# Optimization experiments

Hardware: AMD Instinct MI355X
Metric: run time of the kernel (lower is better)

The kernel has to match this reference:

```python
import jax, jax.numpy as jnp
import numpy as np

B, L, D, H, DFF, MAXD = 4, 2048, 1024, 16, 4096, 512
HD = D // H


def layer_norm(x, gamma, beta, eps=1e-5):
    mu = jnp.mean(x, axis=-1, keepdims=True)
    var = jnp.mean(jnp.square(x - mu), axis=-1, keepdims=True)
    return (x - mu) * jax.lax.rsqrt(var + eps) * gamma + beta


def setup_inputs() -> dict:
    key = jax.random.key(0)
    ks = jax.random.split(key, 8)
    s = 0.02
    return {
        "x": jax.random.normal(ks[0], (B, L, D), jnp.float32),
        "w_qkv": jax.random.normal(ks[1], (D, 3 * D), jnp.float32) * s,
        "w_out": jax.random.normal(ks[2], (D, D), jnp.float32) * s,
        "b_out": jnp.zeros((D,), jnp.float32),
        "bias_table": jax.random.normal(ks[3], (2 * MAXD - 1, H), jnp.float32) * s,
        "gamma1": jnp.ones((D,), jnp.float32),
        "beta1": jnp.zeros((D,), jnp.float32),
        "w_ff1": jax.random.normal(ks[4], (D, DFF), jnp.float32) * s,
        "b_ff1": jnp.zeros((DFF,), jnp.float32),
        "w_ff2": jax.random.normal(ks[5], (DFF, D), jnp.float32) * s,
        "b_ff2": jnp.zeros((D,), jnp.float32),
        "gamma2": jnp.ones((D,), jnp.float32),
        "beta2": jnp.zeros((D,), jnp.float32),
    }


def reference(x, w_qkv, w_out, b_out, bias_table, gamma1, beta1,
              w_ff1, b_ff1, w_ff2, b_ff2, gamma2, beta2):
    b, l, c = x.shape
    scale = HD ** -0.5
    qkv = x @ w_qkv  # [B,L,3D]
    q, k, v = jnp.split(qkv, 3, axis=-1)
    # [B,H,L,hd]
    q = q.reshape(b, l, H, HD).transpose(0, 2, 1, 3)
    k = k.reshape(b, l, H, HD).transpose(0, 2, 1, 3)
    v = v.reshape(b, l, H, HD).transpose(0, 2, 1, 3)
    scores = jnp.einsum("bhqd,bhkd->bhqk", q, k) * scale
    # relative position bias: [H,L,L]
    coords = jnp.arange(l)
    rel = jnp.clip(coords[None, :] - coords[:, None] + MAXD - 1, 0, 2 * MAXD - 2)
    bias = bias_table[rel].transpose(2, 0, 1)
    scores = scores + bias[None]
    attn = jax.nn.softmax(scores, axis=-1)
    ctx = jnp.einsum("bhqk,bhkd->bhqd", attn, v)
    ctx = ctx.transpose(0, 2, 1, 3).reshape(b, l, c)
    attn_out = ctx @ w_out + b_out
    x = layer_norm(x + attn_out, gamma1, beta1)
    h = jax.nn.gelu(x @ w_ff1 + b_ff1, approximate=False)
    ffn_out = h @ w_ff2 + b_ff2
    x = layer_norm(x + ffn_out, gamma2, beta2)
    return x
```

## Files before the change

### kernel.cpp

```cpp
#include <hip/hip_runtime.h>

typedef unsigned short u16;
typedef __bf16 bf16x8 __attribute__((ext_vector_type(8)));
typedef float f32x4 __attribute__((ext_vector_type(4)));
typedef unsigned short u16x8 __attribute__((ext_vector_type(8)));

typedef __attribute__((address_space(1))) const void gvoid_t;
typedef __attribute__((address_space(3))) void svoid_t;

__device__ __forceinline__ float bf2f(u16 u) {
  union { unsigned int i; float f; } v; v.i = ((unsigned int)u) << 16; return v.f;
}
__device__ __forceinline__ u16 f2bf(float f) {
  union { float f; unsigned int i; } v; v.f = f;
  unsigned int u = v.i;
  return (u16)((u + 0x7fffu + ((u >> 16) & 1u)) >> 16);
}
__device__ __forceinline__ void async_copy16(const u16* g, u16* l) {
  __builtin_amdgcn_global_load_lds((gvoid_t*)g, (svoid_t*)l, 16, 0, 0);
}
__device__ __forceinline__ f32x4 mfma16(bf16x8 a, bf16x8 b, f32x4 c) {
  return __builtin_amdgcn_mfma_f32_16x16x32_bf16(a, b, c, 0, 0, 0);
}

__global__ __launch_bounds__(256) void pack_bf16(const float* __restrict__ src, u16* __restrict__ dst, int n4) {
  int i = blockIdx.x * 256 + threadIdx.x;
  if (i >= n4) return;
  float4 v = *(const float4*)(src + (size_t)i * 4);
  ushort4 o;
  o.x = f2bf(v.x); o.y = f2bf(v.y); o.z = f2bf(v.z); o.w = f2bf(v.w);
  *(ushort4*)(dst + (size_t)i * 4) = o;
}

__global__ void transpose_f2b(const float* __restrict__ src, u16* __restrict__ dst, int R, int C) {
  __shared__ u16 t[32][33];
  const int c0 = blockIdx.x * 32, r0 = blockIdx.y * 32;
  const int tx = threadIdx.x, ty = threadIdx.y;
#pragma unroll
  for (int i = 0; i < 4; ++i) {
    int r = r0 + ty + i * 8;
    t[ty + i * 8][tx] = f2bf(src[(size_t)r * C + c0 + tx]);
  }
  __syncthreads();
#pragma unroll
  for (int i = 0; i < 4; ++i) {
    int c = c0 + ty + i * 8;
    dst[(size_t)c * R + r0 + tx] = t[tx][ty + i * 8];
  }
}

__global__ void transpose_v(const u16* __restrict__ qkv, u16* __restrict__ vT2) {
  __shared__ u16 t[32][33];
  const int bh = blockIdx.z;
  const int b = bh >> 4, h = bh & 15;
  const int l0 = blockIdx.x * 32, d0 = blockIdx.y * 32;
  const int tx = threadIdx.x, ty = threadIdx.y;
#pragma unroll
  for (int i = 0; i < 4; ++i) {
    int l = l0 + ty + i * 8;
    t[ty + i * 8][tx] = qkv[(size_t)(b * 2048 + l) * 3072 + 2048 + h * 64 + d0 + tx];
  }
  __syncthreads();
#pragma unroll
  for (int i = 0; i < 4; ++i) {
    int d = d0 + ty + i * 8;
    vT2[(size_t)bh * 131072 + (l0 >> 5) * 2048 + d * 32 + tx] = t[tx][ty + i * 8];
  }
}

template <int EPI>
__global__ __launch_bounds__(256) void gemm_bt(const u16* __restrict__ A, const u16* __restrict__ Bt,
                                               const float* __restrict__ bias, u16* __restrict__ C,
                                               int M, int N, int K) {
  __shared__ __align__(16) u16 As[128 * 32];
  __shared__ __align__(16) u16 Bs[128 * 32];
  const int tid = threadIdx.x;
  const int wave = tid >> 6, lane = tid & 63;
  const int quad = lane >> 4, l16 = lane & 15;
  const int wm = wave >> 1, wn = wave & 1;
  const int m0 = blockIdx.y * 128, n0 = blockIdx.x * 128;
  const int srow = lane >> 2, scol = (lane & 3) * 8;
  f32x4 acc[4][4] = {};
  for (int k0 = 0; k0 < K; k0 += 32) {
#pragma unroll
    for (int rr = 0; rr < 2; ++rr) {
      const int chunk = rr * 4 + wave;
      const int row = chunk * 16 + srow;
      async_copy16(&A[(size_t)(m0 + row) * K + k0 + scol], &As[chunk * 16 * 32]);
      async_copy16(&Bt[(size_t)(n0 + row) * K + k0 + scol], &Bs[chunk * 16 * 32]);
    }
    __syncthreads();
    bf16x8 af[4], bfv[4];
#pragma unroll
    for (int i = 0; i < 4; ++i)
      af[i] = *(const bf16x8*)&As[(wm * 64 + i * 16 + l16) * 32 + quad * 8];
#pragma unroll
    for (int j = 0; j < 4; ++j)
      bfv[j] = *(const bf16x8*)&Bs[(wn * 64 + j * 16 + l16) * 32 + quad * 8];
#pragma unroll
    for (int i = 0; i < 4; ++i)
#pragma unroll
      for (int j = 0; j < 4; ++j)
        acc[i][j] = mfma16(af[i], bfv[j], acc[i][j]);
    __syncthreads();
  }
#pragma unroll
  for (int i = 0; i < 4; ++i)
#pragma unroll
    for (int j = 0; j < 4; ++j) {
      const int col = n0 + wn * 64 + j * 16 + l16;
      float bv = 0.f;
      if (EPI > 0) bv = bias[col];
#pragma unroll
      for (int r = 0; r < 4; ++r) {
        const int row = m0 + wm * 64 + i * 16 + quad * 4 + r;
        float v = acc[i][j][r] + bv;
        if (EPI == 2) v = 0.5f * v * (1.f + erff(v * 0.70710678118654752f));
        C[(size_t)row * N + col] = f2bf(v);
      }
    }
}

__global__ __launch_bounds__(256) void attn_kernel(const u16* __restrict__ qkv, const u16* __restrict__ vT2,
                                                   const float* __restrict__ btab, u16* __restrict__ ctx) {
  const int tid = threadIdx.x;
  const int wave = tid >> 6, lane = tid & 63;
  const int quad = lane >> 4, l16 = lane & 15;
  const int bh = blockIdx.x >> 4, qb = blockIdx.x & 15;
  const int b = bh >> 4, h = bh & 15;
  const int q0b = qb * 128;
  const int qw = q0b + wave * 32;

  __shared__ __align__(16) u16 Ks[32 * 68];
  __shared__ __align__(16) u16 Vs[64 * 36];
  __shared__ __align__(16) float bias_s[160];
  __shared__ __align__(16) u16 P[4][2][16 * 36];

  bf16x8 qf[2][2];
#pragma unroll
  for (int qi = 0; qi < 2; ++qi)
#pragma unroll
    for (int kk = 0; kk < 2; ++kk) {
      const u16* qp = &qkv[((size_t)(b * 2048) + qw + qi * 16 + l16) * 3072 + h * 64 + kk * 32 + quad * 8];
      union { u16 s[8]; bf16x8 v; } u;
#pragma unroll
      for (int j = 0; j < 8; ++j) u.s[j] = f2bf(bf2f(qp[j]) * 0.125f);
      qf[qi][kk] = u.v;
    }

  f32x4 o[2][4] = {};
  float psum[2][4] = {};

  const float c_lo = btab[h], c_hi = btab[1022 * 16 + h];
  const int skey = tid >> 3, schunk = tid & 7;
  const int svd = tid >> 2, svc = tid & 3;

  for (int kt = 0; kt < 64; ++kt) {
    const int kbase = kt * 32;
    const int dmax = kbase - q0b + 31, dmin = kbase - q0b - 127;
    const int mode = (dmax <= -511) ? 1 : (dmin >= 511 ? 2 : 0);
    {
      u16x8 kv = *(const u16x8*)&qkv[((size_t)(b * 2048) + kbase + skey) * 3072 + 1024 + h * 64 + schunk * 8];
      *(u16x8*)&Ks[skey * 68 + schunk * 8] = kv;
      u16x8 vv = *(const u16x8*)&vT2[(size_t)bh * 131072 + kt * 2048 + tid * 8];
      *(u16x8*)&Vs[svd * 36 + svc * 8] = vv;
    }
    if (mode == 0 && tid < 160) {
      int d = dmin + tid + 511;
      d = min(max(d, 0), 1022);
      bias_s[tid] = btab[d * 16 + h];
    }
    __syncthreads();
    bf16x8 kf0[2], kf1[2];
#pragma unroll
    for (int t = 0; t < 2; ++t) {
      kf0[t] = *(const bf16x8*)&Ks[(t * 16 + l16) * 68 + quad * 8];
      kf1[t] = *(const bf16x8*)&Ks[(t * 16 + l16) * 68 + 32 + quad * 8];
    }
#pragma unroll
    for (int qi = 0; qi < 2; ++qi) {
      u16* pw = P[wave][qi];
#pragma unroll
      for (int t = 0; t < 2; ++t) {
        f32x4 z = {0.f, 0.f, 0.f, 0.f};
        z = mfma16(qf[qi][0], kf0[t], z);
        z = mfma16(qf[qi][1], kf1[t], z);
#pragma unroll
        for (int r = 0; r < 4; ++r) {
          float bv;
          if (mode == 1) bv = c_lo;
          else if (mode == 2) bv = c_hi;
          else bv = bias_s[t * 16 + l16 - (wave * 32 + qi * 16 + quad * 4 + r) + 127];
          float p = __expf(z[r] + bv);
          psum[qi][r] += p;
          union { float f; unsigned int i; } cv; cv.f = p;
          pw[(quad * 4 + r) * 36 + t * 16 + l16] = (u16)(cv.i >> 16);
        }
      }
    }
    bf16x8 pa0 = *(const bf16x8*)&P[wave][0][l16 * 36 + quad * 8];
    bf16x8 pa1 = *(const bf16x8*)&P[wave][1][l16 * 36 + quad * 8];
#pragma unroll
    for (int c = 0; c < 4; ++c) {
      bf16x8 vf = *(const bf16x8*)&Vs[(c * 16 + l16) * 36 + quad * 8];
      o[0][c] = mfma16(pa0, vf, o[0][c]);
      o[1][c] = mfma16(pa1, vf, o[1][c]);
    }
    __syncthreads();
  }
#pragma unroll
  for (int qi = 0; qi < 2; ++qi)
#pragma unroll
    for (int off = 1; off < 16; off <<= 1)
#pragma unroll
      for (int r = 0; r < 4; ++r) psum[qi][r] += __shfl_xor(psum[qi][r], off);
#pragma unroll
  for (int qi = 0; qi < 2; ++qi)
#pragma unroll
    for (int r = 0; r < 4; ++r) {
      float inv = 1.f / psum[qi][r];
      int row = qw + qi * 16 + quad * 4 + r;
#pragma unroll
      for (int c = 0; c < 4; ++c)
        ctx[((size_t)(b * 2048 + row)) * 1024 + h * 64 + c * 16 + l16] = f2bf(o[qi][c][r] * inv);
    }
}

template <int A_F32, int O_F32>
__global__ __launch_bounds__(256) void add_ln(const void* __restrict__ av, const u16* __restrict__ b,
                                              const float* __restrict__ gamma, const float* __restrict__ beta,
                                              void* __restrict__ ov) {
  const int row = blockIdx.x, t = threadIdx.x;
  const size_t base = (size_t)row * 1024 + t * 4;
  float x0, x1, x2, x3;
  if (A_F32) {
    float4 a4 = *(const float4*)((const float*)av + base);
    x0 = a4.x; x1 = a4.y; x2 = a4.z; x3 = a4.w;
  } else {
    ushort4 a4 = *(const ushort4*)((const u16*)av + base);
    x0 = bf2f(a4.x); x1 = bf2f(a4.y); x2 = bf2f(a4.z); x3 = bf2f(a4.w);
  }
  ushort4 b4 = *(const ushort4*)&b[base];
  x0 += bf2f(b4.x); x1 += bf2f(b4.y); x2 += bf2f(b4.z); x3 += bf2f(b4.w);
  float s = x0 + x1 + x2 + x3;
  float q = x0 * x0 + x1 * x1 + x2 * x2 + x3 * x3;
  for (int off = 32; off > 0; off >>= 1) { s += __shfl_down(s, off); q += __shfl_down(q, off); }
  __shared__ float sh_s[4], sh_q[4];
  if ((t & 63) == 0) { sh_s[t >> 6] = s; sh_q[t >> 6] = q; }
  __syncthreads();
  s = sh_s[0] + sh_s[1] + sh_s[2] + sh_s[3];
  q = sh_q[0] + sh_q[1] + sh_q[2] + sh_q[3];
  float mu = s * (1.f / 1024.f);
  float var = q * (1.f / 1024.f) - mu * mu;
  float rs = rsqrtf(var + 1e-5f);
  float4 g4 = *(const float4*)&gamma[t * 4];
  float4 be4 = *(const float4*)&beta[t * 4];
  float y0 = (x0 - mu) * rs * g4.x + be4.x;
  float y1 = (x1 - mu) * rs * g4.y + be4.y;
  float y2 = (x2 - mu) * rs * g4.z + be4.z;
  float y3 = (x3 - mu) * rs * g4.w + be4.w;
  if (O_F32) {
    float4 o4 = {y0, y1, y2, y3};
    *(float4*)((float*)ov + base) = o4;
  } else {
    ushort4 o4;
    o4.x = f2bf(y0); o4.y = f2bf(y1); o4.z = f2bf(y2); o4.w = f2bf(y3);
    *(ushort4*)((u16*)ov + base) = o4;
  }
}

extern "C" void kernel_launch(void* const* d_in, const int* in_sizes, int n_in,
                              void* d_out, int out_size, void* d_ws, size_t ws_size,
                              hipStream_t stream) {
  const float* x      = (const float*)d_in[0];
  const float* w_qkv  = (const float*)d_in[1];
  const float* w_out  = (const float*)d_in[2];
  const float* b_out  = (const float*)d_in[3];
  const float* btab   = (const float*)d_in[4];
  const float* gamma1 = (const float*)d_in[5];
  const float* beta1  = (const float*)d_in[6];
  const float* w_ff1  = (const float*)d_in[7];
  const float* b_ff1  = (const float*)d_in[8];
  const float* w_ff2  = (const float*)d_in[9];
  const float* b_ff2  = (const float*)d_in[10];
  const float* gamma2 = (const float*)d_in[11];
  const float* beta2  = (const float*)d_in[12];
  float* out = (float*)d_out;

  char* w = (char*)d_ws;
  auto alloc = [&](size_t elems) { u16* p = (u16*)w; w += elems * 2; return p; };
  u16* wqkvT = alloc(3072UL * 1024);
  u16* woutT = alloc(1024UL * 1024);
  u16* wff1T = alloc(4096UL * 1024);
  u16* wff2T = alloc(1024UL * 4096);
  u16* xb    = alloc(8192UL * 1024);
  u16* qkv   = alloc(8192UL * 3072);
  u16* vT2   = alloc(64UL * 64 * 2048);
  u16* ctx   = alloc(8192UL * 1024);
  u16* x1    = alloc(8192UL * 1024);
  u16* attn  = qkv;
  u16* h     = qkv;
  u16* ffn   = ctx;

  dim3 tb(32, 8);
  pack_bf16<<<8192, 256, 0, stream>>>(x, xb, 8192 * 1024 / 4);
  transpose_f2b<<<dim3(3072 / 32, 1024 / 32), tb, 0, stream>>>(w_qkv, wqkvT, 1024, 3072);
  transpose_f2b<<<dim3(1024 / 32, 1024 / 32), tb, 0, stream>>>(w_out, woutT, 1024, 1024);
  transpose_f2b<<<dim3(4096 / 32, 1024 / 32), tb, 0, stream>>>(w_ff1, wff1T, 1024, 4096);
  transpose_f2b<<<dim3(1024 / 32, 4096 / 32), tb, 0, stream>>>(w_ff2, wff2T, 4096, 1024);

  gemm_bt<0><<<dim3(24, 64), 256, 0, stream>>>(xb, wqkvT, nullptr, qkv, 8192, 3072, 1024);
  transpose_v<<<dim3(64, 2, 64), tb, 0, stream>>>(qkv, vT2);
  attn_kernel<<<1024, 256, 0, stream>>>(qkv, vT2, btab, ctx);
  gemm_bt<1><<<dim3(8, 64), 256, 0, stream>>>(ctx, woutT, b_out, attn, 8192, 1024, 1024);
  add_ln<1, 0><<<8192, 256, 0, stream>>>(x, attn, gamma1, beta1, x1);
  gemm_bt<2><<<dim3(32, 64), 256, 0, stream>>>(x1, wff1T, b_ff1, h, 8192, 4096, 1024);
  gemm_bt<1><<<dim3(8, 64), 256, 0, stream>>>(h, wff2T, b_ff2, ffn, 8192, 1024, 4096);
  add_ln<0, 1><<<8192, 256, 0, stream>>>(x1, ffn, gamma2, beta2, out);
}
```

Before: 640.6 us.

## Widen attention key tile to 64, use exp2 and packed P stores

The attention kernel now processes 64 keys per iteration as two 32-key groups, which halves the number of loop trips and barrier pairs. Q and the bias are prescaled by log2(e) so the exponent can use the hardware exp2, and Q is loaded as one vector instead of scalar loads. The V transpose kernel interleaves key positions so each lane can write two adjacent bf16 probabilities as a single packed 32-bit store into P. Occupancy is hinted with launch_bounds(256,4), and shared-memory padding changes to 72/40 strides. This raises LDS use and register pressure, and the interleaved V layout has to match the packed P column order exactly.

```diff
diff --git a/kernel.cpp b/kernel.cpp
--- a/kernel.cpp
+++ b/kernel.cpp
@@ -61,10 +61,11 @@
     t[ty + i * 8][tx] = qkv[(size_t)(b * 2048 + l) * 3072 + 2048 + h * 64 + d0 + tx];
   }
   __syncthreads();
+  const int pos = 2 * (tx & 15) + (tx >> 4);
 #pragma unroll
   for (int i = 0; i < 4; ++i) {
     int d = d0 + ty + i * 8;
-    vT2[(size_t)bh * 131072 + (l0 >> 5) * 2048 + d * 32 + tx] = t[tx][ty + i * 8];
+    vT2[(size_t)bh * 131072 + (l0 >> 5) * 2048 + d * 32 + pos] = t[tx][ty + i * 8];
   }
 }
 
@@ -121,8 +122,8 @@
     }
 }
 
-__global__ __launch_bounds__(256) void attn_kernel(const u16* __restrict__ qkv, const u16* __restrict__ vT2,
-                                                   const float* __restrict__ btab, u16* __restrict__ ctx) {
+__global__ __launch_bounds__(256, 4) void attn_kernel(const u16* __restrict__ qkv, const u16* __restrict__ vT2,
+                                                      const float* __restrict__ btab, u16* __restrict__ ctx) {
   const int tid = threadIdx.x;
   const int wave = tid >> 6, lane = tid & 63;
   const int quad = lane >> 4, l16 = lane & 15;
@@ -130,81 +131,97 @@
   const int b = bh >> 4, h = bh & 15;
   const int q0b = qb * 128;
   const int qw = q0b + wave * 32;
-
-  __shared__ __align__(16) u16 Ks[32 * 68];
-  __shared__ __align__(16) u16 Vs[64 * 36];
-  __shared__ __align__(16) float bias_s[160];
-  __shared__ __align__(16) u16 P[4][2][16 * 36];
+  const float LOG2E = 1.4426950408889634f;
+
+  __shared__ __align__(16) u16 Ks[64 * 72];
+  __shared__ __align__(16) u16 Vs[2][64 * 40];
+  __shared__ __align__(16) float bias_s[192];
+  __shared__ __align__(16) u16 P[4][2][16 * 40];
 
   bf16x8 qf[2][2];
 #pragma unroll
   for (int qi = 0; qi < 2; ++qi)
 #pragma unroll
     for (int kk = 0; kk < 2; ++kk) {
-      const u16* qp = &qkv[((size_t)(b * 2048) + qw + qi * 16 + l16) * 3072 + h * 64 + kk * 32 + quad * 8];
+      u16x8 qv = *(const u16x8*)&qkv[((size_t)(b * 2048) + qw + qi * 16 + l16) * 3072 + h * 64 + kk * 32 + quad * 8];
       union { u16 s[8]; bf16x8 v; } u;
 #pragma unroll
-      for (int j = 0; j < 8; ++j) u.s[j] = f2bf(bf2f(qp[j]) * 0.125f);
+      for (int j = 0; j < 8; ++j) u.s[j] = f2bf(bf2f(qv[j]) * (0.125f * LOG2E));
       qf[qi][kk] = u.v;
     }
 
   f32x4 o[2][4] = {};
   float psum[2][4] = {};
-
-  const float c_lo = btab[h], c_hi = btab[1022 * 16 + h];
-  const int skey = tid >> 3, schunk = tid & 7;
-  const int svd = tid >> 2, svc = tid & 3;
-
-  for (int kt = 0; kt < 64; ++kt) {
-    const int kbase = kt * 32;
-    const int dmax = kbase - q0b + 31, dmin = kbase - q0b - 127;
+  const float c_lo = btab[h] * LOG2E, c_hi = btab[1022 * 16 + h] * LOG2E;
+  const int krow = tid >> 2, kc = tid & 3;
+  const int rowb0 = wave * 32 + quad * 4;
+
+  for (int kt = 0; kt < 32; ++kt) {
+    const int kbase = kt * 64;
+    const int dmin = kbase - q0b - 127, dmax = kbase - q0b + 63;
     const int mode = (dmax <= -511) ? 1 : (dmin >= 511 ? 2 : 0);
-    {
-      u16x8 kv = *(const u16x8*)&qkv[((size_t)(b * 2048) + kbase + skey) * 3072 + 1024 + h * 64 + schunk * 8];
-      *(u16x8*)&Ks[skey * 68 + schunk * 8] = kv;
-      u16x8 vv = *(const u16x8*)&vT2[(size_t)bh * 131072 + kt * 2048 + tid * 8];
-      *(u16x8*)&Vs[svd * 36 + svc * 8] = vv;
-    }
-    if (mode == 0 && tid < 160) {
-      int d = dmin + tid + 511;
-      d = min(max(d, 0), 1022);
-      bias_s[tid] = btab[d * 16 + h];
+#pragma unroll
+    for (int half = 0; half < 2; ++half) {
+      const int chunk = kc + half * 4;
+      u16x8 kv = *(const u16x8*)&qkv[((size_t)(b * 2048) + kbase + krow) * 3072 + 1024 + h * 64 + chunk * 8];
+      *(u16x8*)&Ks[krow * 72 + chunk * 8] = kv;
+    }
+#pragma unroll
+    for (int g = 0; g < 2; ++g) {
+      u16x8 vv = *(const u16x8*)&vT2[(size_t)bh * 131072 + (2 * kt + g) * 2048 + tid * 8];
+      *(u16x8*)&Vs[g][krow * 40 + kc * 8] = vv;
+    }
+    if (mode == 0 && tid < 192) {
+      int idx = dmin + 191 - tid + 511;
+      idx = min(max(idx, 0), 1022);
+      bias_s[tid] = btab[idx * 16 + h] * LOG2E;
     }
     __syncthreads();
-    bf16x8 kf0[2], kf1[2];
-#pragma unroll
-    for (int t = 0; t < 2; ++t) {
-      kf0[t] = *(const bf16x8*)&Ks[(t * 16 + l16) * 68 + quad * 8];
-      kf1[t] = *(const bf16x8*)&Ks[(t * 16 + l16) * 68 + 32 + quad * 8];
-    }
-#pragma unroll
-    for (int qi = 0; qi < 2; ++qi) {
-      u16* pw = P[wave][qi];
+#pragma unroll
+    for (int g = 0; g < 2; ++g) {
+      f32x4 z[2][2];
 #pragma unroll
       for (int t = 0; t < 2; ++t) {
-        f32x4 z = {0.f, 0.f, 0.f, 0.f};
-        z = mfma16(qf[qi][0], kf0[t], z);
-        z = mfma16(qf[qi][1], kf1[t], z);
-#pragma unroll
-        for (int r = 0; r < 4; ++r) {
-          float bv;
-          if (mode == 1) bv = c_lo;
-          else if (mode == 2) bv = c_hi;
-          else bv = bias_s[t * 16 + l16 - (wave * 32 + qi * 16 + quad * 4 + r) + 127];
-          float p = __expf(z[r] + bv);
-          psum[qi][r] += p;
-          union { float f; unsigned int i; } cv; cv.f = p;
-          pw[(quad * 4 + r) * 36 + t * 16 + l16] = (u16)(cv.i >> 16);
+        const u16* kr = &Ks[(g * 32 + t * 16 + l16) * 72 + quad * 8];
+        bf16x8 kf0 = *(const bf16x8*)kr;
+        bf16x8 kf1 = *(const bf16x8*)(kr + 32);
+#pragma unroll
+        for (int qi = 0; qi < 2; ++qi) {
+          f32x4 zz = {0.f, 0.f, 0.f, 0.f};
+          zz = mfma16(qf[qi][0], kf0, zz);
+          zz = mfma16(qf[qi][1], kf1, zz);
+          z[t][qi] = zz;
         }
       }
-    }
-    bf16x8 pa0 = *(const bf16x8*)&P[wave][0][l16 * 36 + quad * 8];
-    bf16x8 pa1 = *(const bf16x8*)&P[wave][1][l16 * 36 + quad * 8];
-#pragma unroll
-    for (int c = 0; c < 4; ++c) {
-      bf16x8 vf = *(const bf16x8*)&Vs[(c * 16 + l16) * 36 + quad * 8];
-      o[0][c] = mfma16(pa0, vf, o[0][c]);
-      o[1][c] = mfma16(pa1, vf, o[1][c]);
+#pragma unroll
+      for (int qi = 0; qi < 2; ++qi) {
+        u16* pw = P[wave][qi];
+#pragma unroll
+        for (int r = 0; r < 4; ++r) {
+          const int rowb = rowb0 + qi * 16 + r;
+          float b0, b1;
+          if (mode == 1) { b0 = c_lo; b1 = c_lo; }
+          else if (mode == 2) { b0 = c_hi; b1 = c_hi; }
+          else {
+            b0 = bias_s[64 + rowb - (g * 32 + l16)];
+            b1 = bias_s[48 + rowb - (g * 32 + l16)];
+          }
+          float p0 = __builtin_amdgcn_exp2f(z[0][qi][r] + b0);
+          float p1 = __builtin_amdgcn_exp2f(z[1][qi][r] + b1);
+          psum[qi][r] += p0 + p1;
+          union { float f; unsigned u; } a0, a1; a0.f = p0; a1.f = p1;
+          unsigned pk = __builtin_amdgcn_perm(a1.u, a0.u, 0x07060302u);
+          *(unsigned*)&pw[(quad * 4 + r) * 40 + 2 * l16] = pk;
+        }
+      }
+      bf16x8 pa0 = *(const bf16x8*)&P[wave][0][l16 * 40 + quad * 8];
+      bf16x8 pa1 = *(const bf16x8*)&P[wave][1][l16 * 40 + quad * 8];
+#pragma unroll
+      for (int c = 0; c < 4; ++c) {
+        bf16x8 vf = *(const bf16x8*)&Vs[g][(c * 16 + l16) * 40 + quad * 8];
+        o[0][c] = mfma16(pa0, vf, o[0][c]);
+        o[1][c] = mfma16(pa1, vf, o[1][c]);
+      }
     }
     __syncthreads();
   }
```

Result: faster. 608.5 us (-5.0%).
